# Kernel tuning notes

Hardware: AMD Instinct MI355X
Metric: run time of the kernel (lower is better)

## Reference

```python
import jax, jax.numpy as jnp
import numpy as np

H, DK, DV = 16, 128, 128
BINS = 64
EPS = 1e-6
NORM_EPS = 1e-5


def silu(x):
    return x * jax.nn.sigmoid(x)


def short_conv(x, w):
    # causal depthwise conv over time + silu. x: [B,T,C], w: [C,K]
    C = x.shape[-1]
    K = w.shape[1]
    lhs = jnp.swapaxes(x, 1, 2)              # [B,C,T]
    rhs = w[:, None, :]                      # [C,1,K]
    out = jax.lax.conv_general_dilated(
        lhs, rhs, window_strides=(1,), padding=[(K - 1, 0)],
        dimension_numbers=('NCH', 'OIH', 'NCH'), feature_group_count=C)
    return silu(jnp.swapaxes(out, 1, 2))


def delta_rule(q, k, v, beta, decay):
    # gated delta-rule linear attention recurrence.
    # q,k: [B,T,H,DK], v: [B,T,H,DV], beta: [B,T,H], decay: [B,T,H,DK]
    B = q.shape[0]

    def step(S, inp):
        qt, kt, vt, bt, gt = inp             # [B,H,DK],...,[B,H],[B,H,DK]
        Sd = S * gt[..., None]               # per-key-channel decay
        v_pred = jnp.einsum('bhk,bhkv->bhv', kt, Sd)
        S_new = Sd + jnp.einsum('bhk,bhv->bhkv', kt * bt[..., None], vt - v_pred)
        ot = jnp.einsum('bhk,bhkv->bhv', qt, S_new)
        return S_new, ot

    tm = lambda a: jnp.swapaxes(a, 0, 1)     # time-major
    S0 = jnp.zeros((B, H, DK, DV), q.dtype)
    _, o = jax.lax.scan(step, S0, (tm(q), tm(k), tm(v), tm(beta), tm(decay)))
    return jnp.swapaxes(o, 0, 1)             # [B,T,H,DV]


def _forward(hidden_states, wq, wk, wv, conv_q_w, conv_k_w, conv_v_w, A_log, dt_bias,
             proxy_w, unc_w, head_embed, mlp_w1, mlp_b1, mlp_w2, mlp_b2,
             bb_w, bb_b, bd_w, bd_b, lam_w, lam_b, ab_w, ab_b, ad_w, ad_b,
             g1_w, g2_w, g2_b, onorm_w, wo):
    x = hidden_states
    B, T, _ = x.shape
    q = short_conv(x @ wq, conv_q_w).reshape(B, T, H, DK)
    k = short_conv(x @ wk, conv_k_w).reshape(B, T, H, DK)
    v = short_conv(x @ wv, conv_v_w).reshape(B, T, H, DV)

    # uncertainty (entropy of predicted-token distribution proxy)
    logp = jax.nn.log_softmax(x @ unc_w, axis=-1)
    entropy = -jnp.sum(jnp.exp(logp) * logp, axis=-1)              # [B,T]
    ent_norm = entropy / jnp.log(jnp.asarray(BINS, x.dtype))

    # beta-norm: unit-norm keys inside the kernel
    k_unit = k / (jnp.linalg.norm(k, axis=-1, keepdims=True) + EPS)

    # proxy-value surprise features, per head/token
    v_hat = jnp.einsum('bthk,kv->bthv', k, proxy_w)
    err = v - v_hat
    err_n = jnp.linalg.norm(err, axis=-1)                          # [B,T,H]
    v_n = jnp.linalg.norm(v, axis=-1)
    vh_n = jnp.linalg.norm(v_hat, axis=-1)
    rel_err = err_n / (v_n + EPS)
    cos = jnp.sum(v * v_hat, axis=-1) / (v_n * vh_n + EPS)
    feats = jnp.stack([jnp.broadcast_to(ent_norm[..., None], err_n.shape),
                       rel_err, cos, jnp.log1p(err_n)], axis=-1)    # [B,T,H,4]
    he = jnp.broadcast_to(head_embed[None, None], (B, T, H, head_embed.shape[-1]))
    feats = jnp.concatenate([feats, he], axis=-1)                   # [B,T,H,8]

    hf = silu(silu(feats @ mlp_w1 + mlp_b1) @ mlp_w2 + mlp_b2)      # [B,T,H,32]
    beta_base = hf @ bb_w + bb_b[0]
    beta_delta = hf @ bd_w + bd_b[0]
    beta_fast = jax.nn.sigmoid(beta_base + beta_delta)              # fast memory: bigger step
    beta_slow = jax.nn.sigmoid(beta_base - beta_delta)              # slow memory: smaller step
    lam = jax.nn.sigmoid(hf @ lam_w + lam_b[0])                     # mixing gate
    amp_base = hf @ ab_w + ab_b[0]
    amp_delta = hf @ ad_w + ad_b[0]
    amp_fast = jax.nn.sigmoid(amp_base + amp_delta)
    amp_slow = jax.nn.sigmoid(amp_base - amp_delta)

    # KDA-style per-key-channel log-decay: g = -exp(A_log) * softplus(dt_bias)
    g_chan = -jnp.exp(A_log)[:, None] * jax.nn.softplus(dt_bias).reshape(H, DK)
    decay_fast = jnp.exp(g_chan[None, None] * amp_fast[..., None])  # [B,T,H,DK]
    decay_slow = jnp.exp(g_chan[None, None] * amp_slow[..., None])

    qs = q * (DK ** -0.5)
    o_fast = delta_rule(qs, k_unit, v, beta_fast, decay_fast)
    o_slow = delta_rule(qs, k_unit, v, beta_slow, decay_slow)
    o = lam[..., None] * o_fast + (1.0 - lam[..., None]) * o_slow   # [B,T,H,DV]

    # gated RMSNorm (sigmoid gate) + output projection
    g = ((x @ g1_w) @ g2_w + g2_b).reshape(B, T, H, DV)
    rms = jnp.sqrt(jnp.mean(o * o, axis=-1, keepdims=True) + NORM_EPS)
    o = (o / rms) * onorm_w * jax.nn.sigmoid(g)
    return o.reshape(B, T, H * DV) @ wo


def setup_inputs() -> dict:
    key = jax.random.key(0)
    ks = jax.random.split(key, 40)
    B, T, D = 2, 256, 2048

    def w(k, shape, fan_in):
        return jax.random.normal(k, shape, jnp.float32) * (fan_in ** -0.5)

    return {
        'hidden_states': jax.random.normal(ks[0], (B, T, D), jnp.float32),
        'wq': w(ks[1], (D, H * DK), D),
        'wk': w(ks[2], (D, H * DK), D),
        'wv': w(ks[3], (D, H * DV), D),
        'conv_q_w': w(ks[4], (H * DK, 4), 4),
        'conv_k_w': w(ks[5], (H * DK, 4), 4),
        'conv_v_w': w(ks[6], (H * DV, 4), 4),
        'A_log': jnp.log(jax.random.uniform(ks[7], (H,), jnp.float32, 1.0, 16.0)),
        'dt_bias': jnp.zeros((H * DK,), jnp.float32),
        'proxy_w': w(ks[8], (DK, DV), DK),
        'unc_w': w(ks[9], (D, BINS), D),
        'head_embed': jax.random.normal(ks[10], (H, 4), jnp.float32),
        'mlp_w1': w(ks[11], (8, 32), 8),
        'mlp_b1': jnp.zeros((32,), jnp.float32),
        'mlp_w2': w(ks[12], (32, 32), 32),
        'mlp_b2': jnp.zeros((32,), jnp.float32),
        'bb_w': w(ks[13], (32,), 32), 'bb_b': jnp.zeros((1,), jnp.float32),
        'bd_w': w(ks[14], (32,), 32), 'bd_b': jnp.zeros((1,), jnp.float32),
        'lam_w': w(ks[15], (32,), 32), 'lam_b': jnp.zeros((1,), jnp.float32),
        'ab_w': w(ks[16], (32,), 32), 'ab_b': jnp.zeros((1,), jnp.float32),
        'ad_w': w(ks[17], (32,), 32), 'ad_b': jnp.zeros((1,), jnp.float32),
        'g1_w': w(ks[18], (D, DV), D),
        'g2_w': w(ks[19], (DV, H * DV), DV),
        'g2_b': jnp.zeros((H * DV,), jnp.float32),
        'onorm_w': jnp.ones((DV,), jnp.float32),
        'wo': w(ks[20], (H * DV, D), H * DV),
    }


def reference(hidden_states, wq, wk, wv, conv_q_w, conv_k_w, conv_v_w, A_log, dt_bias,
              proxy_w, unc_w, head_embed, mlp_w1, mlp_b1, mlp_w2, mlp_b2,
              bb_w, bb_b, bd_w, bd_b, lam_w, lam_b, ab_w, ab_b, ad_w, ad_b,
              g1_w, g2_w, g2_b, onorm_w, wo):
    return _forward(hidden_states, wq, wk, wv, conv_q_w, conv_k_w, conv_v_w, A_log,
                    dt_bias, proxy_w, unc_w, head_embed, mlp_w1, mlp_b1, mlp_w2, mlp_b2,
                    bb_w, bb_b, bd_w, bd_b, lam_w, lam_b, ab_w, ab_b, ad_w, ad_b,
                    g1_w, g2_w, g2_b, onorm_w, wo)
```

## Files before the change

kernel.cpp:

```cpp
#include <hip/hip_runtime.h>
#include <hip/hip_bf16.h>
#include <math.h>

#define H_ 16
#define DK_ 128
#define DV_ 128
#define D_ 2048
#define T_ 256
#define B_ 2
#define BT_ 512

typedef __attribute__((ext_vector_type(8))) short short8v;
typedef __attribute__((ext_vector_type(4))) float float4v;
typedef unsigned short ushort_t;

__device__ __forceinline__ float sigmoidf_(float x){ return 1.f/(1.f+expf(-x)); }
__device__ __forceinline__ float siluf_(float x){ return x/(1.f+expf(-x)); }
__device__ __forceinline__ ushort_t f2bf(float f){
    __hip_bfloat16 h = __float2bfloat16(f);
    return *reinterpret_cast<ushort_t*>(&h);
}
__device__ __forceinline__ int swz(int row, int k){
    return row * 32 + ((((k >> 3) ^ (row & 3)) << 3) | (k & 7));
}

template<int CTRL>
__device__ __forceinline__ float ror_add_(float x){
    return x + __int_as_float(__builtin_amdgcn_update_dpp(
        0, __float_as_int(x), CTRL, 0xF, 0xF, true));
}
__device__ __forceinline__ float rsum16_(float x){
    x = ror_add_<0x121>(x);
    x = ror_add_<0x122>(x);
    x = ror_add_<0x124>(x);
    x = ror_add_<0x128>(x);
    return x;
}

__global__ void cvt_bf16(const float* __restrict__ in, ushort_t* __restrict__ out, int n){
    int i = (blockIdx.x * 256 + threadIdx.x) * 4;
    if (i >= n) return;
    float4 v = *(const float4*)&in[i];
    union { ushort_t s[4]; unsigned long long u; } p;
    p.s[0] = f2bf(v.x); p.s[1] = f2bf(v.y); p.s[2] = f2bf(v.z); p.s[3] = f2bf(v.w);
    *(unsigned long long*)&out[i] = p.u;
}

__global__ void gchan_k(const float* __restrict__ A_log, const float* __restrict__ dt_bias,
                        float* __restrict__ gchan)
{
    int i = blockIdx.x * 256 + threadIdx.x;
    int h = i >> 7;
    float x = dt_bias[i];
    float sp = (x > 20.f) ? x : log1pf(expf(x));
    gchan[i] = -expf(A_log[h]) * sp * 1.44269504088896f;
}

__device__ __forceinline__ void gemm_core(
    const ushort_t* __restrict__ A, int K,
    const float* __restrict__ W, int Nst, int nloc0,
    float* __restrict__ C, int Cst, int m0, int n0out)
{
    __shared__ ushort_t Asub[2048];
    __shared__ ushort_t Bsub[2048];
    const int tid = threadIdx.x;
    const int wid = tid >> 6, lane = tid & 63;
    const int wr = (wid >> 1) * 32, wc = (wid & 1) * 32;
    const int lr = lane & 15, lk = (lane >> 4) * 8;
    const int rowA = tid >> 2, kqA = tid & 3;
    const int nW = tid & 63, kqW = tid >> 6;

    float4v acc[2][2];
    #pragma unroll
    for (int i = 0; i < 2; ++i)
        #pragma unroll
        for (int j = 0; j < 2; ++j) acc[i][j] = (float4v){0.f, 0.f, 0.f, 0.f};

    short8v aRa, aRb;
    float wRa[8], wRb[8];

#define LOADT(AR, WR, KOFF) do {                                                   \
    AR = *(const short8v*)&A[(size_t)(m0 + rowA) * K + (KOFF) + kqA * 8];          \
    _Pragma("unroll")                                                              \
    for (int r = 0; r < 8; ++r)                                                    \
        WR[r] = W[(size_t)((KOFF) + kqW * 8 + r) * Nst + nloc0 + nW];              \
} while (0)
#define STORET(AR, WR) do {                                                        \
    *(short8v*)&Asub[swz(rowA, kqA * 8)] = AR;                                     \
    union { ushort_t s[8]; short8v v; } pk;                                        \
    _Pragma("unroll")                                                              \
    for (int r = 0; r < 8; ++r) pk.s[r] = f2bf(WR[r]);                             \
    *(short8v*)&Bsub[swz(nW, kqW * 8)] = pk.v;                                     \
} while (0)
#define FRAGMMA() do {                                                             \
    short8v af0 = *(const short8v*)&Asub[swz(wr + lr, lk)];                        \
    short8v af1 = *(const short8v*)&Asub[swz(wr + 16 + lr, lk)];                   \
    short8v bf0 = *(const short8v*)&Bsub[swz(wc + lr, lk)];                        \
    short8v bf1 = *(const short8v*)&Bsub[swz(wc + 16 + lr, lk)];                   \
    acc[0][0] = __builtin_amdgcn_mfma_f32_16x16x32_bf16(af0, bf0, acc[0][0],0,0,0);\
    acc[0][1] = __builtin_amdgcn_mfma_f32_16x16x32_bf16(af0, bf1, acc[0][1],0,0,0);\
    acc[1][0] = __builtin_amdgcn_mfma_f32_16x16x32_bf16(af1, bf0, acc[1][0],0,0,0);\
    acc[1][1] = __builtin_amdgcn_mfma_f32_16x16x32_bf16(af1, bf1, acc[1][1],0,0,0);\
} while (0)

    LOADT(aRa, wRa, 0);
    for (int k0 = 0; k0 < K; k0 += 64) {
        STORET(aRa, wRa);
        __syncthreads();
        if (k0 + 32 < K) LOADT(aRb, wRb, k0 + 32);
        FRAGMMA();
        __syncthreads();
        STORET(aRb, wRb);
        __syncthreads();
        if (k0 + 64 < K) LOADT(aRa, wRa, k0 + 64);
        FRAGMMA();
        __syncthreads();
    }
#undef LOADT
#undef STORET
#undef FRAGMMA
    const int lq = (lane >> 4) * 4;
    #pragma unroll
    for (int mi = 0; mi < 2; ++mi)
        #pragma unroll
        for (int ni = 0; ni < 2; ++ni)
            #pragma unroll
            for (int j = 0; j < 4; ++j)
                C[(size_t)(m0 + wr + mi * 16 + lq + j) * Cst + (n0out + wc + ni * 16 + lr)]
                    = acc[mi][ni][j];
}

__device__ __forceinline__ void gemm_core2(
    const ushort_t* __restrict__ A, int K,
    const float* __restrict__ W, int Nst, int nloc0,
    float* __restrict__ C, int Cst, int m0, int n0out)
{
    __shared__ ushort_t Asub[8192];
    __shared__ ushort_t Bsub[2048];
    const int tid = threadIdx.x;
    const int wid = tid >> 6, lane = tid & 63;
    const int wr = wid * 32;
    const int lr = lane & 15, lk = (lane >> 4) * 8;
    const int rowA = tid >> 2;
    const int kqA  = (tid & 3) * 8;
    const int nW = tid & 63, kqW = (tid >> 6) & 3;
    const bool doW = tid < 256;

    float4v acc[2][4];
    #pragma unroll
    for (int i = 0; i < 2; ++i)
        #pragma unroll
        for (int j = 0; j < 4; ++j) acc[i][j] = (float4v){0.f, 0.f, 0.f, 0.f};

    short8v a0a, a1a, a0b, a1b;
    float wRa[8], wRb[8];

#define LOADT2(A0, A1, WR, KOFF) do {                                              \
    A0 = *(const short8v*)&A[(size_t)(m0 + rowA) * K + (KOFF) + kqA];              \
    A1 = *(const short8v*)&A[(size_t)(m0 + rowA + 128) * K + (KOFF) + kqA];        \
    if (doW) {                                                                     \
        _Pragma("unroll")                                                          \
        for (int r = 0; r < 8; ++r)                                                \
            WR[r] = W[(size_t)((KOFF) + kqW * 8 + r) * Nst + nloc0 + nW];          \
    }                                                                              \
} while (0)
#define STORET2(A0, A1, WR) do {                                                   \
    *(short8v*)&Asub[swz(rowA, kqA)] = A0;                                         \
    *(short8v*)&Asub[swz(rowA + 128, kqA)] = A1;                                   \
    if (doW) {                                                                     \
        union { ushort_t s[8]; short8v v; } pk;                                    \
        _Pragma("unroll")                                                          \
        for (int r = 0; r < 8; ++r) pk.s[r] = f2bf(WR[r]);                         \
        *(short8v*)&Bsub[swz(nW, kqW * 8)] = pk.v;                                 \
    }                                                                              \
} while (0)
#define FRAGMMA2() do {                                                            \
    short8v af0 = *(const short8v*)&Asub[swz(wr + lr, lk)];                        \
    short8v af1 = *(const short8v*)&Asub[swz(wr + 16 + lr, lk)];                   \
    short8v bf0 = *(const short8v*)&Bsub[swz(lr, lk)];                             \
    short8v bf1 = *(const short8v*)&Bsub[swz(16 + lr, lk)];                        \
    short8v bf2 = *(const short8v*)&Bsub[swz(32 + lr, lk)];                        \
    short8v bf3 = *(const short8v*)&Bsub[swz(48 + lr, lk)];                        \
    acc[0][0] = __builtin_amdgcn_mfma_f32_16x16x32_bf16(af0, bf0, acc[0][0],0,0,0);\
    acc[0][1] = __builtin_amdgcn_mfma_f32_16x16x32_bf16(af0, bf1, acc[0][1],0,0,0);\
    acc[0][2] = __builtin_amdgcn_mfma_f32_16x16x32_bf16(af0, bf2, acc[0][2],0,0,0);\
    acc[0][3] = __builtin_amdgcn_mfma_f32_16x16x32_bf16(af0, bf3, acc[0][3],0,0,0);\
    acc[1][0] = __builtin_amdgcn_mfma_f32_16x16x32_bf16(af1, bf0, acc[1][0],0,0,0);\
    acc[1][1] = __builtin_amdgcn_mfma_f32_16x16x32_bf16(af1, bf1, acc[1][1],0,0,0);\
    acc[1][2] = __builtin_amdgcn_mfma_f32_16x16x32_bf16(af1, bf2, acc[1][2],0,0,0);\
    acc[1][3] = __builtin_amdgcn_mfma_f32_16x16x32_bf16(af1, bf3, acc[1][3],0,0,0);\
} while (0)

    LOADT2(a0a, a1a, wRa, 0);
    for (int k0 = 0; k0 < K; k0 += 64) {
        STORET2(a0a, a1a, wRa);
        __syncthreads();
        if (k0 + 32 < K) LOADT2(a0b, a1b, wRb, k0 + 32);
        FRAGMMA2();
        __syncthreads();
        STORET2(a0b, a1b, wRb);
        __syncthreads();
        if (k0 + 64 < K) LOADT2(a0a, a1a, wRa, k0 + 64);
        FRAGMMA2();
        __syncthreads();
    }
#undef LOADT2
#undef STORET2
#undef FRAGMMA2
    const int lq = (lane >> 4) * 4;
    #pragma unroll
    for (int mi = 0; mi < 2; ++mi)
        #pragma unroll
        for (int ni = 0; ni < 4; ++ni)
            #pragma unroll
            for (int j = 0; j < 4; ++j)
                C[(size_t)(m0 + wr + mi * 16 + lq + j) * Cst + (n0out + ni * 16 + lr)]
                    = acc[mi][ni][j];
}

__global__ __launch_bounds__(512) void gemm_proj(const ushort_t* __restrict__ A,
    const float* __restrict__ wq, const float* __restrict__ wk, const float* __restrict__ wv,
    const float* __restrict__ unc, const float* __restrict__ g1, float* __restrict__ C)
{
    int n0 = blockIdx.x * 64, m0 = blockIdx.y * 256;
    const float* W; int nloc, Nst;
    if (n0 < 2048)      { W = wq;  nloc = n0;        Nst = 2048; }
    else if (n0 < 4096) { W = wk;  nloc = n0 - 2048; Nst = 2048; }
    else if (n0 < 6144) { W = wv;  nloc = n0 - 4096; Nst = 2048; }
    else if (n0 < 6208) { W = unc; nloc = n0 - 6144; Nst = 64; }
    else                { W = g1;  nloc = n0 - 6208; Nst = 128; }
    gemm_core2(A, 2048, W, Nst, nloc, C, 6336, m0, n0);
}

__global__ __launch_bounds__(256) void gemm_one(const ushort_t* __restrict__ A,
    const float* __restrict__ W, float* __restrict__ C, int N, int K)
{
    gemm_core(A, K, W, N, blockIdx.x * 64, C, N, blockIdx.y * 64, blockIdx.x * 64);
}

__global__ __launch_bounds__(256) void gemm_g2(const float* __restrict__ Cb,
    const float* __restrict__ W, float* __restrict__ C)
{
    __shared__ ushort_t Asub[2048];
    __shared__ ushort_t Bsub[2048];
    const int tid = threadIdx.x;
    const int wid = tid >> 6, lane = tid & 63;
    const int wr = (wid >> 1) * 32, wc = (wid & 1) * 32;
    const int lr = lane & 15, lk = (lane >> 4) * 8;
    const int rowA = tid >> 2, kqA = (tid & 3) * 8;
    const int nW = tid & 63, kqW = tid >> 6;
    const int m0 = blockIdx.y * 64, n0 = blockIdx.x * 64;

    float4v acc[2][2];
    #pragma unroll
    for (int i = 0; i < 2; ++i)
        #pragma unroll
        for (int j = 0; j < 2; ++j) acc[i][j] = (float4v){0.f, 0.f, 0.f, 0.f};

    for (int k0 = 0; k0 < 128; k0 += 32) {
        const float* asrc = &Cb[(size_t)(m0 + rowA) * 6336 + 6208 + k0 + kqA];
        float4 a4a = *(const float4*)asrc;
        float4 a4b = *(const float4*)(asrc + 4);
        float w8[8];
        #pragma unroll
        for (int r = 0; r < 8; ++r)
            w8[r] = W[(size_t)(k0 + kqW * 8 + r) * 2048 + n0 + nW];
        __syncthreads();
        union { ushort_t s[8]; short8v v; } pa, pw;
        pa.s[0]=f2bf(a4a.x); pa.s[1]=f2bf(a4a.y); pa.s[2]=f2bf(a4a.z); pa.s[3]=f2bf(a4a.w);
        pa.s[4]=f2bf(a4b.x); pa.s[5]=f2bf(a4b.y); pa.s[6]=f2bf(a4b.z); pa.s[7]=f2bf(a4b.w);
        *(short8v*)&Asub[swz(rowA, kqA)] = pa.v;
        #pragma unroll
        for (int r = 0; r < 8; ++r) pw.s[r] = f2bf(w8[r]);
        *(short8v*)&Bsub[swz(nW, kqW * 8)] = pw.v;
        __syncthreads();
        short8v af0 = *(const short8v*)&Asub[swz(wr + lr, lk)];
        short8v af1 = *(const short8v*)&Asub[swz(wr + 16 + lr, lk)];
        short8v bf0 = *(const short8v*)&Bsub[swz(wc + lr, lk)];
        short8v bf1 = *(const short8v*)&Bsub[swz(wc + 16 + lr, lk)];
        acc[0][0] = __builtin_amdgcn_mfma_f32_16x16x32_bf16(af0, bf0, acc[0][0],0,0,0);
        acc[0][1] = __builtin_amdgcn_mfma_f32_16x16x32_bf16(af0, bf1, acc[0][1],0,0,0);
        acc[1][0] = __builtin_amdgcn_mfma_f32_16x16x32_bf16(af1, bf0, acc[1][0],0,0,0);
        acc[1][1] = __builtin_amdgcn_mfma_f32_16x16x32_bf16(af1, bf1, acc[1][1],0,0,0);
    }
    const int lq = (lane >> 4) * 4;
    #pragma unroll
    for (int mi = 0; mi < 2; ++mi)
        #pragma unroll
        for (int ni = 0; ni < 2; ++ni)
            #pragma unroll
            for (int j = 0; j < 4; ++j)
                C[(size_t)(m0 + wr + mi * 16 + lq + j) * 2048 + (n0 + wc + ni * 16 + lr)]
                    = acc[mi][ni][j];
}

__global__ void conv_fused(const float* __restrict__ Cb,
    const float* __restrict__ wq, const float* __restrict__ wk, const float* __restrict__ wv,
    float* __restrict__ qc, float* __restrict__ kc, float* __restrict__ vc,
    ushort_t* __restrict__ kcb, float qscale)
{
    int c  = blockIdx.x * 256 + threadIdx.x;
    int bt = blockIdx.y;
    int b  = bt / T_, t = bt % T_;
    int which = c >> 11, cloc = c & 2047;
    const float* w = which == 0 ? wq : which == 1 ? wk : wv;
    float* o = which == 0 ? qc : which == 1 ? kc : vc;
    float scale = which == 0 ? qscale : 1.f;
    float acc = 0.f;
    #pragma unroll
    for (int j = 0; j < 4; ++j) {
        int tt = t - 3 + j;
        if (tt >= 0) acc = fmaf(w[cloc * 4 + j], Cb[((size_t)(b * T_ + tt)) * 6336 + c], acc);
    }
    float r = siluf_(acc) * scale;
    o[(size_t)bt * D_ + cloc] = r;
    if (which == 1) kcb[(size_t)bt * D_ + cloc] = f2bf(r);
}

__global__ __launch_bounds__(128) void featsprec_k(
    const float* __restrict__ kc, const float* __restrict__ vc,
    const float* __restrict__ qc,
    const float* __restrict__ vhatA, const float* __restrict__ Cb,
    const float* __restrict__ he, const float* __restrict__ gchan,
    const float* __restrict__ w1, const float* __restrict__ b1,
    const float* __restrict__ w2, const float* __restrict__ b2,
    const float* __restrict__ bbw, const float* __restrict__ bbb,
    const float* __restrict__ bdw, const float* __restrict__ bdb,
    const float* __restrict__ lamw, const float* __restrict__ lamb,
    const float* __restrict__ abw, const float* __restrict__ abb,
    const float* __restrict__ adw, const float* __restrict__ adb,
    float* __restrict__ lm, float* __restrict__ kuA,
    float* __restrict__ dA, float4* __restrict__ scal4A)
{
    int blk = blockIdx.x;
    int h = blk & 15, bt = blk >> 4;
    int b = bt / T_, t = bt % T_;
    int v = threadIdx.x;
    __shared__ float part[2][5];
    __shared__ float tot5[5];
    __shared__ float feats8[8];
    __shared__ float hf1[32];
    __shared__ float hf[32];
    __shared__ float entSh;
    __shared__ float scal5[5];

    if (v < 64) {
        float x = Cb[(size_t)bt * 6336 + 6144 + v];
        float m = x;
        #pragma unroll
        for (int o = 32; o > 0; o >>= 1) m = fmaxf(m, __shfl_xor(m, o));
        float e = expf(x - m);
        float s = e;
        #pragma unroll
        for (int o = 32; o > 0; o >>= 1) s += __shfl_xor(s, o);
        float lp = (x - m) - logf(s);
        float c = -expf(lp) * lp;
        #pragma unroll
        for (int o = 32; o > 0; o >>= 1) c += __shfl_xor(c, o);
        if (v == 0) entSh = c / logf(64.f);
    }

    size_t base = (size_t)bt * D_ + h * 128;
    float kval = kc[base + v];
    float vval = vc[base + v];
    float vhat = vhatA[(size_t)blk * 128 + v];

    float e = vval - vhat;
    float sums[5] = {kval * kval, vval * vval, vhat * vhat, vval * vhat, e * e};
    #pragma unroll
    for (int i = 0; i < 5; ++i) {
        float s = sums[i];
        #pragma unroll
        for (int o = 32; o > 0; o >>= 1) s += __shfl_xor(s, o);
        if ((threadIdx.x & 63) == 0) part[threadIdx.x >> 6][i] = s;
    }
    __syncthreads();
    if (threadIdx.x < 5) tot5[threadIdx.x] = part[0][threadIdx.x] + part[1][threadIdx.x];
    __syncthreads();
    if (threadIdx.x == 0) {
        float k2 = tot5[0], v2 = tot5[1], vh2 = tot5[2], vvh = tot5[3], e2 = tot5[4];
        float knorm = sqrtf(k2);
        float err_n = sqrtf(e2);
        float v_n = sqrtf(v2);
        float vh_n = sqrtf(vh2);
        feats8[0] = entSh;
        feats8[1] = err_n / (v_n + 1e-6f);
        feats8[2] = vvh / (v_n * vh_n + 1e-6f);
        feats8[3] = log1pf(err_n);
        feats8[4] = he[h * 4 + 0];
        feats8[5] = he[h * 4 + 1];
        feats8[6] = he[h * 4 + 2];
        feats8[7] = he[h * 4 + 3];
        scal5[4] = knorm;
    }
    __syncthreads();
    if (threadIdx.x < 32) {
        float a = b1[threadIdx.x];
        #pragma unroll
        for (int j = 0; j < 8; ++j) a = fmaf(feats8[j], w1[j * 32 + threadIdx.x], a);
        hf1[threadIdx.x] = siluf_(a);
    }
    __syncthreads();
    if (threadIdx.x < 32) {
        float a = b2[threadIdx.x];
        #pragma unroll
        for (int j = 0; j < 32; ++j) a = fmaf(hf1[j], w2[j * 32 + threadIdx.x], a);
        hf[threadIdx.x] = siluf_(a);
    }
    __syncthreads();
    if (threadIdx.x == 0) {
        float bb = bbb[0], bd = bdb[0], lv = lamb[0], ab = abb[0], ad = adb[0];
        #pragma unroll
        for (int j = 0; j < 32; ++j) {
            float hj = hf[j];
            bb = fmaf(hj, bbw[j], bb);
            bd = fmaf(hj, bdw[j], bd);
            lv = fmaf(hj, lamw[j], lv);
            ab = fmaf(hj, abw[j], ab);
            ad = fmaf(hj, adw[j], ad);
        }
        scal5[0] = sigmoidf_(bb + bd);
        scal5[1] = sigmoidf_(bb - bd);
        scal5[2] = sigmoidf_(ab + ad);
        scal5[3] = sigmoidf_(ab - ad);
        lm[((size_t)(b * H_ + h)) * T_ + t] = sigmoidf_(lv);
    }
    __syncthreads();

    const float bfv = scal5[0], bsv = scal5[1];
    const float afv = scal5[2], asv = scal5[3], knv = scal5[4];
    const int k = threadIdx.x;
    const int bh = b * 16 + h;
    float gch = gchan[h * 128 + k];
    float kuv = kval / (knv + 1e-6f);
    kuA[((size_t)bh * 256 + t) * 128 + k] = kuv;
    dA[((size_t)bh * 256 + t) * 128 + k]        = exp2f(gch * afv);
    dA[((size_t)(32 + bh) * 256 + t) * 128 + k] = exp2f(gch * asv);
    float pq = qc[base + k] * kuv;
    #pragma unroll
    for (int o = 32; o > 0; o >>= 1) pq += __shfl_xor(pq, o);
    if ((threadIdx.x & 63) == 0) part[threadIdx.x >> 6][0] = pq;
    __syncthreads();
    if (threadIdx.x == 0) {
        float pt = part[0][0] + part[1][0];
        float4 s0; s0.x = afv; s0.y = bfv; s0.z = pt * bfv; s0.w = 0.f;
        float4 s1; s1.x = asv; s1.y = bsv; s1.z = pt * bsv; s1.w = 0.f;
        scal4A[(size_t)bh * 256 + t] = s0;
        scal4A[(size_t)(32 + bh) * 256 + t] = s1;
    }
}

struct OPS { float4 a0, a1, q0, q1, d0, d1, sc; float2 vv; };

__global__ __launch_bounds__(256) void delta_wave9(
    const float* __restrict__ qc, const float* __restrict__ vc,
    const float* __restrict__ kuA, const float* __restrict__ dA,
    const float4* __restrict__ scal4A,
    float* __restrict__ o_fast, float* __restrict__ o_slow)
{
    const int p  = blockIdx.x;
    const int lb = (p & 7) * 32 + (p >> 3);
    const int bh = lb >> 3, rule = (lb >> 2) & 1, vq = lb & 3;
    const int b = bh >> 4, h = bh & 15;
    const int rbh = rule * 32 + bh;
    const int tid = threadIdx.x;
    const int wid = tid >> 6, lane = tid & 63;
    const int kl = lane & 15, vg = lane >> 4;
    const int vloc = wid * 8 + vg * 2;
    const int vcol = vq * 32 + vloc;

    __shared__ float kuL[2][16][144];
    __shared__ float qL [2][16][144];
    __shared__ float dL [2][16][144];
    __shared__ float vL [2][16][32];
    __shared__ float scL[2][16][4];

    const float*  __restrict__ pkuG = kuA + (size_t)bh * 256 * 128;
    const float*  __restrict__ pdG  = dA + (size_t)rbh * 256 * 128;
    const float*  __restrict__ pqG  = qc + (size_t)b * T_ * D_ + h * 128;
    const float*  __restrict__ pvG  = vc + (size_t)b * T_ * D_ + h * 128 + vq * 32;
    const float4* __restrict__ pscG = scal4A + (size_t)rbh * 256;
    float* __restrict__ obase = (rule ? o_slow : o_fast)
                                + (size_t)b * T_ * D_ + h * 128 + vcol;

    const int srow = (tid & 127) >> 3;
    const int scol = (tid & 7) * 16;
    const bool isK = tid < 128;
    const int ck0 = scol >> 3;
    const int fo_w0 = ck0 * 8 + (ck0 >> 2) * 4;
    const int fo_w1 = (ck0 + 1) * 8 + ((ck0 + 1) >> 2) * 4;

    float4 sb0, sb1, sb2, sb3, svb, ssc, sd0, sd1;

    float S[8][2];
    #pragma unroll
    for (int j = 0; j < 8; ++j) { S[j][0] = 0.f; S[j][1] = 0.f; }

#define STAGE_LOAD(C) do {                                                         \
    const int t0_ = (C) * 16;                                                      \
    const float* dsrc = pdG + (size_t)(t0_ + srow) * 128 + scol;                   \
    if (isK) {                                                                     \
        const float* src = pkuG + (size_t)(t0_ + srow) * 128 + scol;               \
        sb0 = *(const float4*)(src);      sb1 = *(const float4*)(src + 4);         \
        sb2 = *(const float4*)(src + 8);  sb3 = *(const float4*)(src + 12);        \
        svb = *(const float4*)(pvG + (size_t)(t0_ + srow) * D_ + (tid & 7) * 4);   \
        sd0 = *(const float4*)(dsrc);     sd1 = *(const float4*)(dsrc + 4);        \
    } else {                                                                       \
        const float* src = pqG + (size_t)(t0_ + srow) * D_ + scol;                 \
        sb0 = *(const float4*)(src);      sb1 = *(const float4*)(src + 4);         \
        sb2 = *(const float4*)(src + 8);  sb3 = *(const float4*)(src + 12);        \
        sd0 = *(const float4*)(dsrc + 8); sd1 = *(const float4*)(dsrc + 12);       \
        if ((tid & 127) < 16) ssc = *(const float4*)&pscG[t0_ + (tid & 127)];      \
    }                                                                              \
} while (0)

#define STAGE_WRITE(BI) do {                                                       \
    if (isK) {                                                                     \
        *(float4*)&kuL[BI][srow][fo_w0]     = sb0;                                 \
        *(float4*)&kuL[BI][srow][fo_w0 + 4] = sb1;                                 \
        *(float4*)&kuL[BI][srow][fo_w1]     = sb2;                                 \
        *(float4*)&kuL[BI][srow][fo_w1 + 4] = sb3;                                 \
        *(float4*)&vL[BI][srow][(tid & 7) * 4] = svb;                              \
        *(float4*)&dL[BI][srow][fo_w0]      = sd0;                                 \
        *(float4*)&dL[BI][srow][fo_w0 + 4]  = sd1;                                 \
    } else {                                                                       \
        *(float4*)&qL[BI][srow][fo_w0]     = sb0;                                  \
        *(float4*)&qL[BI][srow][fo_w0 + 4] = sb1;                                  \
        *(float4*)&qL[BI][srow][fo_w1]     = sb2;                                  \
        *(float4*)&qL[BI][srow][fo_w1 + 4] = sb3;                                  \
        *(float4*)&dL[BI][srow][fo_w1]      = sd0;                                 \
        *(float4*)&dL[BI][srow][fo_w1 + 4]  = sd1;                                 \
        if ((tid & 127) < 16) *(float4*)&scL[BI][tid & 127][0] = ssc;              \
    }                                                                              \
} while (0)

#define LDOPS(R, BI, TS) do {                                                      \
    R.a0 = *(const float4*)&kuL[BI][TS][fo];                                       \
    R.a1 = *(const float4*)&kuL[BI][TS][fo + 4];                                   \
    R.q0 = *(const float4*)&qL[BI][TS][fo];                                        \
    R.q1 = *(const float4*)&qL[BI][TS][fo + 4];                                    \
    R.d0 = *(const float4*)&dL[BI][TS][fo];                                        \
    R.d1 = *(const float4*)&dL[BI][TS][fo + 4];                                    \
    R.vv = *(const float2*)&vL[BI][TS][vloc];                                      \
    R.sc = *(const float4*)&scL[BI][TS][0];                                        \
} while (0)

#define STEP(TT, CUR, NXT, BI) do {                                                \
    if ((TT) + 1 < 16) LDOPS(NXT, BI, (TT) + 1);                                   \
    float ku[8] = {CUR.a0.x, CUR.a0.y, CUR.a0.z, CUR.a0.w,                         \
                   CUR.a1.x, CUR.a1.y, CUR.a1.z, CUR.a1.w};                        \
    float qv[8] = {CUR.q0.x, CUR.q0.y, CUR.q0.z, CUR.q0.w,                         \
                   CUR.q1.x, CUR.q1.y, CUR.q1.z, CUR.q1.w};                        \
    float d[8]  = {CUR.d0.x, CUR.d0.y, CUR.d0.z, CUR.d0.w,                         \
                   CUR.d1.x, CUR.d1.y, CUR.d1.z, CUR.d1.w};                        \
    float vp0a = 0.f, vp0b = 0.f, vp1a = 0.f, vp1b = 0.f;                          \
    float oq0a = 0.f, oq0b = 0.f, oq1a = 0.f, oq1b = 0.f;                          \
    _Pragma("unroll")                                                              \
    for (int j = 0; j < 4; ++j) {                                                  \
        float kudA = ku[j] * d[j],     qdA = qv[j] * d[j];                         \
        float kudB = ku[j+4] * d[j+4], qdB = qv[j+4] * d[j+4];                     \
        vp0a = fmaf(kudA, S[j][0], vp0a);   vp0b = fmaf(kudB, S[j+4][0], vp0b);    \
        vp1a = fmaf(kudA, S[j][1], vp1a);   vp1b = fmaf(kudB, S[j+4][1], vp1b);    \
        oq0a = fmaf(qdA,  S[j][0], oq0a);   oq0b = fmaf(qdB,  S[j+4][0], oq0b);    \
        oq1a = fmaf(qdA,  S[j][1], oq1a);   oq1b = fmaf(qdB,  S[j+4][1], oq1b);    \
    }                                                                              \
    float vp0 = rsum16_(vp0a + vp0b);                                              \
    float vp1 = rsum16_(vp1a + vp1b);                                              \
    float oq0 = rsum16_(oq0a + oq0b);                                              \
    float oq1 = rsum16_(oq1a + oq1b);                                              \
    float dv0 = CUR.vv.x - vp0, dv1 = CUR.vv.y - vp1;                              \
    float o0 = fmaf(CUR.sc.z, dv0, oq0);                                           \
    float o1 = fmaf(CUR.sc.z, dv1, oq1);                                           \
    float bd0 = CUR.sc.y * dv0, bd1 = CUR.sc.y * dv1;                              \
    _Pragma("unroll")                                                              \
    for (int j = 0; j < 8; ++j) {                                                  \
        S[j][0] = fmaf(d[j], S[j][0], ku[j] * bd0);                                \
        S[j][1] = fmaf(d[j], S[j][1], ku[j] * bd1);                                \
    }                                                                              \
    if (kl == 0) {                                                                 \
        float2 ov; ov.x = o0; ov.y = o1;                                           \
        *(float2*)&obase[(size_t)(tb + (TT)) * D_] = ov;                           \
    }                                                                              \
} while (0)

    const int fo = kl * 8 + (kl >> 2) * 4;

    STAGE_LOAD(0);
    STAGE_WRITE(0);
    __syncthreads();

    OPS rA, rB;
    for (int c = 0; c < 16; ++c) {
        if (c < 15) STAGE_LOAD(c + 1);
        const int bi = c & 1;
        const int tb = c * 16;
        LDOPS(rA, bi, 0);
        #pragma unroll
        for (int ts = 0; ts < 16; ts += 2) {
            STEP(ts,     rA, rB, bi);
            STEP(ts + 1, rB, rA, bi);
        }
        if (c < 15) STAGE_WRITE((c + 1) & 1);
        __syncthreads();
    }
#undef STAGE_LOAD
#undef STAGE_WRITE
#undef LDOPS
#undef STEP
}

__global__ __launch_bounds__(128) void combine_k(
    const float* __restrict__ of, const float* __restrict__ os,
    const float* __restrict__ lm, const float* __restrict__ graw,
    const float* __restrict__ g2b, const float* __restrict__ onw,
    ushort_t* __restrict__ ocb)
{
    int blk = blockIdx.x;
    int h = blk & 15, bt = blk >> 4;
    int b = bt / T_, t = bt % T_;
    int v = threadIdx.x;
    size_t idx = (size_t)bt * D_ + h * 128 + v;
    float l = lm[((size_t)(b * H_ + h)) * T_ + t];
    float o = l * of[idx] + (1.f - l) * os[idx];
    float s = o * o;
    #pragma unroll
    for (int off = 32; off > 0; off >>= 1) s += __shfl_xor(s, off);
    __shared__ float ws2[2];
    if ((threadIdx.x & 63) == 0) ws2[threadIdx.x >> 6] = s;
    __syncthreads();
    float tot = ws2[0] + ws2[1];
    float rms = sqrtf(tot / 128.f + 1e-5f);
    float g = graw[idx] + g2b[h * 128 + v];
    ocb[idx] = f2bf(o / rms * onw[v] * sigmoidf_(g));
}

extern "C" void kernel_launch(void* const* d_in, const int* in_sizes, int n_in,
                              void* d_out, int out_size, void* d_ws, size_t ws_size,
                              hipStream_t stream)
{
    const float* x        = (const float*)d_in[0];
    const float* wq       = (const float*)d_in[1];
    const float* wk       = (const float*)d_in[2];
    const float* wv       = (const float*)d_in[3];
    const float* conv_q_w = (const float*)d_in[4];
    const float* conv_k_w = (const float*)d_in[5];
    const float* conv_v_w = (const float*)d_in[6];
    const float* A_log    = (const float*)d_in[7];
    const float* dt_bias  = (const float*)d_in[8];
    const float* proxy_w  = (const float*)d_in[9];
    const float* unc_w    = (const float*)d_in[10];
    const float* he       = (const float*)d_in[11];
    const float* mlp_w1   = (const float*)d_in[12];
    const float* mlp_b1   = (const float*)d_in[13];
    const float* mlp_w2   = (const float*)d_in[14];
    const float* mlp_b2   = (const float*)d_in[15];
    const float* bb_w     = (const float*)d_in[16];
    const float* bb_b     = (const float*)d_in[17];
    const float* bd_w     = (const float*)d_in[18];
    const float* bd_b     = (const float*)d_in[19];
    const float* lam_w    = (const float*)d_in[20];
    const float* lam_b    = (const float*)d_in[21];
    const float* ab_w     = (const float*)d_in[22];
    const float* ab_b     = (const float*)d_in[23];
    const float* ad_w     = (const float*)d_in[24];
    const float* ad_b     = (const float*)d_in[25];
    const float* g1_w     = (const float*)d_in[26];
    const float* g2_w     = (const float*)d_in[27];
    const float* g2_b     = (const float*)d_in[28];
    const float* onorm_w  = (const float*)d_in[29];
    const float* wo       = (const float*)d_in[30];
    float* out = (float*)d_out;

    float* ws = (float*)d_ws;
    const size_t SZ = (size_t)BT_ * D_;
    float* C_big = ws;
    float* qc    = C_big + (size_t)512 * 6336;
    float* kc    = qc + SZ;
    float* vc    = kc + SZ;
    float* graw  = vc + SZ;
    float* lm    = graw + SZ;
    float* gchan = lm + 8192;
    float* scal4 = gchan + 2048;
    float* kuA   = scal4 + 65536;
    float* dA    = kuA + 1048576;
    float* vhatA = dA + 2097152;
    float* fend  = vhatA + 1048576;
    ushort_t* xb = (ushort_t*)fend;

    float* o_fast  = C_big;
    float* o_slow  = C_big + SZ;
    ushort_t* ocb  = xb;
    ushort_t* kcb  = (ushort_t*)dA;

    dim3 blk256(256);
    dim3 blk512(512);
    const float QSCALE = 0.08838834764831845f;

    cvt_bf16<<<dim3(1024), blk256, 0, stream>>>(x, xb, (int)SZ);
    gemm_proj<<<dim3(99, 2), blk512, 0, stream>>>(xb, wq, wk, wv, unc_w, g1_w, C_big);
    gemm_g2<<<dim3(32, 8), blk256, 0, stream>>>(C_big, g2_w, graw);
    conv_fused<<<dim3(24, BT_), blk256, 0, stream>>>(C_big, conv_q_w, conv_k_w, conv_v_w,
                                                     qc, kc, vc, kcb, QSCALE);
    gemm_one<<<dim3(2, 128), blk256, 0, stream>>>(kcb, proxy_w, vhatA, 128, 128);
    gchan_k<<<dim3(8), blk256, 0, stream>>>(A_log, dt_bias, gchan);
    featsprec_k<<<dim3(BT_ * H_), dim3(128), 0, stream>>>(
        kc, vc, qc, vhatA, C_big, he, gchan,
        mlp_w1, mlp_b1, mlp_w2, mlp_b2,
        bb_w, bb_b, bd_w, bd_b, lam_w, lam_b, ab_w, ab_b, ad_w, ad_b,
        lm, kuA, dA, (float4*)scal4);
    delta_wave9<<<dim3(256), blk256, 0, stream>>>(qc, vc, kuA, dA,
                                                  (const float4*)scal4,
                                                  o_fast, o_slow);
    combine_k<<<dim3(BT_ * H_), dim3(128), 0, stream>>>(o_fast, o_slow, lm, graw,
                                                        g2_b, onorm_w, ocb);
    gemm_one<<<dim3(32, 8), blk256, 0, stream>>>(ocb, wo, out, 2048, 2048);
}
```

Baseline: 212.7 us.

## Recompute decay and unit keys inside recurrence kernel instead of materializing them

The feature kernel no longer writes per-timestep unit-norm keys and per-channel decay tensors (about 3M floats) to global memory. The recurrence kernel now reads raw conv keys and the norm packed into the scalar record, and computes the unit keys and the decay factors with exp2f in registers while staging each chunk. The gchan kernel is also merged into the bf16 conversion launch, saving one launch. The cost is extra exp2f and a reciprocal inside the latency-sensitive recurrence staging path.

Result: slower. 219.5 us (+3.2%).

```diff
diff --git a/kernel.cpp b/kernel.cpp
--- a/kernel.cpp
+++ b/kernel.cpp
@@ -37,23 +37,25 @@
     return x;
 }
 
-__global__ void cvt_bf16(const float* __restrict__ in, ushort_t* __restrict__ out, int n){
-    int i = (blockIdx.x * 256 + threadIdx.x) * 4;
-    if (i >= n) return;
-    float4 v = *(const float4*)&in[i];
-    union { ushort_t s[4]; unsigned long long u; } p;
-    p.s[0] = f2bf(v.x); p.s[1] = f2bf(v.y); p.s[2] = f2bf(v.z); p.s[3] = f2bf(v.w);
-    *(unsigned long long*)&out[i] = p.u;
-}
-
-__global__ void gchan_k(const float* __restrict__ A_log, const float* __restrict__ dt_bias,
-                        float* __restrict__ gchan)
-{
-    int i = blockIdx.x * 256 + threadIdx.x;
-    int h = i >> 7;
-    float x = dt_bias[i];
-    float sp = (x > 20.f) ? x : log1pf(expf(x));
-    gchan[i] = -expf(A_log[h]) * sp * 1.44269504088896f;
+__global__ void cvt_gchan(const float* __restrict__ in, ushort_t* __restrict__ out, int n,
+                          const float* __restrict__ A_log, const float* __restrict__ dt_bias,
+                          float* __restrict__ gchan)
+{
+    int bid = blockIdx.x;
+    if (bid < 1024) {
+        int i = (bid * 256 + threadIdx.x) * 4;
+        if (i >= n) return;
+        float4 v = *(const float4*)&in[i];
+        union { ushort_t s[4]; unsigned long long u; } p;
+        p.s[0] = f2bf(v.x); p.s[1] = f2bf(v.y); p.s[2] = f2bf(v.z); p.s[3] = f2bf(v.w);
+        *(unsigned long long*)&out[i] = p.u;
+    } else {
+        int i = (bid - 1024) * 256 + threadIdx.x;
+        int h = i >> 7;
+        float x = dt_bias[i];
+        float sp = (x > 20.f) ? x : log1pf(expf(x));
+        gchan[i] = -expf(A_log[h]) * sp * 1.44269504088896f;
+    }
 }
 
 __device__ __forceinline__ void gemm_core(
@@ -321,7 +323,7 @@
     const float* __restrict__ kc, const float* __restrict__ vc,
     const float* __restrict__ qc,
     const float* __restrict__ vhatA, const float* __restrict__ Cb,
-    const float* __restrict__ he, const float* __restrict__ gchan,
+    const float* __restrict__ he,
     const float* __restrict__ w1, const float* __restrict__ b1,
     const float* __restrict__ w2, const float* __restrict__ b2,
     const float* __restrict__ bbw, const float* __restrict__ bbb,
@@ -329,8 +331,7 @@
     const float* __restrict__ lamw, const float* __restrict__ lamb,
     const float* __restrict__ abw, const float* __restrict__ abb,
     const float* __restrict__ adw, const float* __restrict__ adb,
-    float* __restrict__ lm, float* __restrict__ kuA,
-    float* __restrict__ dA, float4* __restrict__ scal4A)
+    float* __restrict__ lm, float4* __restrict__ scal4A)
 {
     int blk = blockIdx.x;
     int h = blk & 15, bt = blk >> 4;
@@ -431,11 +432,7 @@
     const float afv = scal5[2], asv = scal5[3], knv = scal5[4];
     const int k = threadIdx.x;
     const int bh = b * 16 + h;
-    float gch = gchan[h * 128 + k];
     float kuv = kval / (knv + 1e-6f);
-    kuA[((size_t)bh * 256 + t) * 128 + k] = kuv;
-    dA[((size_t)bh * 256 + t) * 128 + k]        = exp2f(gch * afv);
-    dA[((size_t)(32 + bh) * 256 + t) * 128 + k] = exp2f(gch * asv);
     float pq = qc[base + k] * kuv;
     #pragma unroll
     for (int o = 32; o > 0; o >>= 1) pq += __shfl_xor(pq, o);
@@ -443,8 +440,8 @@
     __syncthreads();
     if (threadIdx.x == 0) {
         float pt = part[0][0] + part[1][0];
-        float4 s0; s0.x = afv; s0.y = bfv; s0.z = pt * bfv; s0.w = 0.f;
-        float4 s1; s1.x = asv; s1.y = bsv; s1.z = pt * bsv; s1.w = 0.f;
+        float4 s0; s0.x = afv; s0.y = bfv; s0.z = pt * bfv; s0.w = knv;
+        float4 s1; s1.x = asv; s1.y = bsv; s1.z = pt * bsv; s1.w = knv;
         scal4A[(size_t)bh * 256 + t] = s0;
         scal4A[(size_t)(32 + bh) * 256 + t] = s1;
     }
@@ -452,9 +449,9 @@
 
 struct OPS { float4 a0, a1, q0, q1, d0, d1, sc; float2 vv; };
 
-__global__ __launch_bounds__(256) void delta_wave9(
+__global__ __launch_bounds__(256) void delta_wave10(
     const float* __restrict__ qc, const float* __restrict__ vc,
-    const float* __restrict__ kuA, const float* __restrict__ dA,
+    const float* __restrict__ kc, const float* __restrict__ gchan,
     const float4* __restrict__ scal4A,
     float* __restrict__ o_fast, float* __restrict__ o_slow)
 {
@@ -475,8 +472,7 @@
     __shared__ float vL [2][16][32];
     __shared__ float scL[2][16][4];
 
-    const float*  __restrict__ pkuG = kuA + (size_t)bh * 256 * 128;
-    const float*  __restrict__ pdG  = dA + (size_t)rbh * 256 * 128;
+    const float*  __restrict__ pkcG = kc + (size_t)b * T_ * D_ + h * 128;
     const float*  __restrict__ pqG  = qc + (size_t)b * T_ * D_ + h * 128;
     const float*  __restrict__ pvG  = vc + (size_t)b * T_ * D_ + h * 128 + vq * 32;
     const float4* __restrict__ pscG = scal4A + (size_t)rbh * 256;
@@ -490,6 +486,13 @@
     const int fo_w0 = ck0 * 8 + (ck0 >> 2) * 4;
     const int fo_w1 = (ck0 + 1) * 8 + ((ck0 + 1) >> 2) * 4;
 
+    float gchr[8];
+    {
+        const int gbase = h * 128 + scol + (isK ? 0 : 8);
+        #pragma unroll
+        for (int j = 0; j < 8; ++j) gchr[j] = gchan[gbase + j];
+    }
+
     float4 sb0, sb1, sb2, sb3, svb, ssc, sd0, sd1;
 
     float S[8][2];
@@ -498,18 +501,26 @@
 
 #define STAGE_LOAD(C) do {                                                         \
     const int t0_ = (C) * 16;                                                      \
-    const float* dsrc = pdG + (size_t)(t0_ + srow) * 128 + scol;                   \
+    float4 rowsc = pscG[t0_ + srow];                                               \
+    float amp_ = rowsc.x;                                                          \
+    float rkn_ = 1.f / (rowsc.w + 1e-6f);                                          \
+    sd0.x = exp2f(gchr[0] * amp_); sd0.y = exp2f(gchr[1] * amp_);                  \
+    sd0.z = exp2f(gchr[2] * amp_); sd0.w = exp2f(gchr[3] * amp_);                  \
+    sd1.x = exp2f(gchr[4] * amp_); sd1.y = exp2f(gchr[5] * amp_);                  \
+    sd1.z = exp2f(gchr[6] * amp_); sd1.w = exp2f(gchr[7] * amp_);                  \
     if (isK) {                                                                     \
-        const float* src = pkuG + (size_t)(t0_ + srow) * 128 + scol;               \
+        const float* src = pkcG + (size_t)(t0_ + srow) * D_ + scol;                \
         sb0 = *(const float4*)(src);      sb1 = *(const float4*)(src + 4);         \
         sb2 = *(const float4*)(src + 8);  sb3 = *(const float4*)(src + 12);        \
+        sb0.x *= rkn_; sb0.y *= rkn_; sb0.z *= rkn_; sb0.w *= rkn_;                \
+        sb1.x *= rkn_; sb1.y *= rkn_; sb1.z *= rkn_; sb1.w *= rkn_;                \
+        sb2.x *= rkn_; sb2.y *= rkn_; sb2.z *= rkn_; sb2.w *= rkn_;                \
+        sb3.x *= rkn_; sb3.y *= rkn_; sb3.z *= rkn_; sb3.w *= rkn_;                \
         svb = *(const float4*)(pvG + (size_t)(t0_ + srow) * D_ + (tid & 7) * 4);   \
-        sd0 = *(const float4*)(dsrc);     sd1 = *(const float4*)(dsrc + 4);        \
     } else {                                                                       \
         const float* src = pqG + (size_t)(t0_ + srow) * D_ + scol;                 \
         sb0 = *(const float4*)(src);      sb1 = *(const float4*)(src + 4);         \
         sb2 = *(const float4*)(src + 8);  sb3 = *(const float4*)(src + 12);        \
-        sd0 = *(const float4*)(dsrc + 8); sd1 = *(const float4*)(dsrc + 12);       \
         if ((tid & 127) < 16) ssc = *(const float4*)&pscG[t0_ + (tid & 127)];      \
     }                                                                              \
 } while (0)
@@ -681,36 +692,34 @@
     float* lm    = graw + SZ;
     float* gchan = lm + 8192;
     float* scal4 = gchan + 2048;
-    float* kuA   = scal4 + 65536;
-    float* dA    = kuA + 1048576;
-    float* vhatA = dA + 2097152;
+    float* kcbF  = scal4 + 65536;
+    float* vhatA = kcbF + 524288;
     float* fend  = vhatA + 1048576;
     ushort_t* xb = (ushort_t*)fend;
 
     float* o_fast  = C_big;
     float* o_slow  = C_big + SZ;
     ushort_t* ocb  = xb;
-    ushort_t* kcb  = (ushort_t*)dA;
+    ushort_t* kcb  = (ushort_t*)kcbF;
 
     dim3 blk256(256);
     dim3 blk512(512);
     const float QSCALE = 0.08838834764831845f;
 
-    cvt_bf16<<<dim3(1024), blk256, 0, stream>>>(x, xb, (int)SZ);
+    cvt_gchan<<<dim3(1032), blk256, 0, stream>>>(x, xb, (int)SZ, A_log, dt_bias, gchan);
     gemm_proj<<<dim3(99, 2), blk512, 0, stream>>>(xb, wq, wk, wv, unc_w, g1_w, C_big);
     gemm_g2<<<dim3(32, 8), blk256, 0, stream>>>(C_big, g2_w, graw);
     conv_fused<<<dim3(24, BT_), blk256, 0, stream>>>(C_big, conv_q_w, conv_k_w, conv_v_w,
                                                      qc, kc, vc, kcb, QSCALE);
     gemm_one<<<dim3(2, 128), blk256, 0, stream>>>(kcb, proxy_w, vhatA, 128, 128);
-    gchan_k<<<dim3(8), blk256, 0, stream>>>(A_log, dt_bias, gchan);
     featsprec_k<<<dim3(BT_ * H_), dim3(128), 0, stream>>>(
-        kc, vc, qc, vhatA, C_big, he, gchan,
+        kc, vc, qc, vhatA, C_big, he,
         mlp_w1, mlp_b1, mlp_w2, mlp_b2,
         bb_w, bb_b, bd_w, bd_b, lam_w, lam_b, ab_w, ab_b, ad_w, ad_b,
-        lm, kuA, dA, (float4*)scal4);
-    delta_wave9<<<dim3(256), blk256, 0, stream>>>(qc, vc, kuA, dA,
-                                                  (const float4*)scal4,
-                                                  o_fast, o_slow);
+        lm, (float4*)scal4);
+    delta_wave10<<<dim3(256), blk256, 0, stream>>>(qc, vc, kc, gchan,
+                                                   (const float4*)scal4,
+                                                   o_fast, o_slow);
     combine_k<<<dim3(BT_ * H_), dim3(128), 0, stream>>>(o_fast, o_slow, lm, graw,
                                                         g2_b, onorm_w, ocb);
     gemm_one<<<dim3(32, 8), blk256, 0, stream>>>(ocb, wo, out, 2048, 2048);
```
